# Kernel tuning notes

Hardware: AMD Instinct MI355X
Metric: run time of the kernel (lower is better)

## Reference

```python
import jax, jax.numpy as jnp
import numpy as np

N = 40000      # nodes
E = 640000     # edges
G = 2048       # graphs
D = 128        # emb_dim
T = 10         # num_tasks
L = 5          # layers
ATOM_VOCAB = 64
BOND_VOCAB = 8
BN_EPS = 1e-5


def _bn(x, g, b, m, v):
    # inference-mode BatchNorm1d with running stats
    return (x - m) * jax.lax.rsqrt(v + BN_EPS) * g + b


def setup_inputs() -> dict:
    key = jax.random.key(0)
    ks = jax.random.split(key, 24)
    inp = {
        "x_atom": jax.random.randint(ks[0], (N, 9), 0, ATOM_VOCAB),
        "edge_index": jax.random.randint(ks[1], (2, E), 0, N),
        "edge_attr": jax.random.randint(ks[2], (E, 3), 0, BOND_VOCAB),
        "batch": jnp.sort(jax.random.randint(ks[3], (N,), 0, G)),
        # embedding tables
        "atom_emb": jax.random.normal(ks[4], (9, ATOM_VOCAB, D)) * 0.1,
        "bond_emb": jax.random.normal(ks[5], (L, 3, BOND_VOCAB, D)) * 0.1,
        # per-layer GIN params (stacked over L)
        "eps": jnp.zeros((L,)),
        "W1": jax.random.normal(ks[6], (L, D, 2 * D)) * 0.05,
        "b1": jnp.zeros((L, 2 * D)),
        "g1": jnp.ones((L, 2 * D)),
        "bt1": jnp.zeros((L, 2 * D)),
        "m1": jax.random.normal(ks[7], (L, 2 * D)) * 0.1,
        "v1": jax.random.uniform(ks[8], (L, 2 * D), minval=0.5, maxval=1.5),
        "W2": jax.random.normal(ks[9], (L, 2 * D, D)) * 0.05,
        "b2": jnp.zeros((L, D)),
        # outer BatchNorm per layer
        "gO": jnp.ones((L, D)),
        "btO": jnp.zeros((L, D)),
        "mO": jax.random.normal(ks[10], (L, D)) * 0.1,
        "vO": jax.random.uniform(ks[11], (L, D), minval=0.5, maxval=1.5),
        # prediction head
        "Wp": jax.random.normal(ks[12], (D, T)) * 0.05,
        "bp": jnp.zeros((T,)),
    }
    return inp


def reference(x_atom, edge_index, edge_attr, batch, atom_emb, bond_emb, eps,
              W1, b1, g1, bt1, m1, v1, W2, b2, gO, btO, mO, vO, Wp, bp):
    src, dst = edge_index[0], edge_index[1]
    # AtomEncoder: sum of per-feature embeddings -> [N, D]
    x = atom_emb[jnp.arange(9)[None, :], x_atom].sum(axis=1)
    feat3 = jnp.arange(3)[None, :]
    for i in range(L):
        # BondEncoder for this layer -> [E, D]
        e = bond_emb[i][feat3, edge_attr].sum(axis=1)
        # message: relu(x_j + edge_emb); aggregate: scatter-add at dst
        msg = jax.nn.relu(x[src] + e)
        agg = jax.ops.segment_sum(msg, dst, num_segments=N)
        h = (1.0 + eps[i]) * x + agg
        # MLP: Linear -> BN -> ReLU -> Linear
        h = jax.nn.relu(_bn(h @ W1[i] + b1[i], g1[i], bt1[i], m1[i], v1[i]))
        h = h @ W2[i] + b2[i]
        # outer BN; ReLU after all but last layer (dropout = identity in eval)
        x = _bn(h, gO[i], btO[i], mO[i], vO[i])
        if i < L - 1:
            x = jax.nn.relu(x)
    # global mean pool over graphs
    sums = jax.ops.segment_sum(x, batch, num_segments=G)
    cnt = jax.ops.segment_sum(jnp.ones((N,), x.dtype), batch, num_segments=G)
    pooled = sums / jnp.maximum(cnt, 1.0)[:, None]
    return pooled @ Wp + bp
```

## Files before the change

### kernel.cpp

```cpp
#include <hip/hip_runtime.h>
#include <hip/hip_bf16.h>

#define NN 40000
#define NE 640000
#define NG 2048
#define DD 128
#define NT 10
#define NL 5
#define NB 80

typedef __attribute__((ext_vector_type(8))) short short8;
typedef __attribute__((ext_vector_type(4))) float f32x4;
typedef unsigned short ushort_t;

static __device__ __forceinline__ ushort_t f2b(float f) {
    return __bfloat16_as_ushort(__float2bfloat16(f));
}
static __device__ __forceinline__ float b2f(ushort_t u) {
    return __bfloat162float(__ushort_as_bfloat16(u));
}

__global__ void __launch_bounds__(256)
k_setup(const float* __restrict__ W1, const float* __restrict__ W2,
        const float* __restrict__ bemb, const int* __restrict__ xa,
        const float* __restrict__ aemb, const int* __restrict__ ei,
        ushort_t* __restrict__ W1P, ushort_t* __restrict__ W2P,
        ushort_t* __restrict__ ebsum16, ushort_t* __restrict__ x16,
        int* __restrict__ deg) {
    int b = blockIdx.x, t = threadIdx.x;
    if (b < 1280) {
        int tid = b * 256 + t;
        int layer = tid >> 16;
        int r = tid & 65535;
        int half = r >> 15;
        int q = r & 32767;
        int j = q & 7;
        int lane = (q >> 3) & 63;
        if (half == 0) {
            int kk = (q >> 9) & 3;
            int nt = q >> 11;
            int n = nt * 16 + (lane & 15);
            int k = kk * 32 + (lane >> 4) * 8 + j;
            W1P[layer * 32768 + q] = f2b(W1[(layer * DD + k) * 256 + n]);
        } else {
            int kk = (q >> 9) & 7;
            int nt = q >> 12;
            int n = nt * 16 + (lane & 15);
            int k = kk * 32 + (lane >> 4) * 8 + j;
            W2P[layer * 32768 + q] = f2b(W2[(layer * 256 + k) * DD + n]);
        }
        int d = tid & 127;
        int c = (tid >> 7) & 511;
        const float* bl = bemb + (size_t)layer * 3 * 8 * DD;
        ebsum16[tid] = f2b(bl[(c & 7) * DD + d] + bl[(8 + ((c >> 3) & 7)) * DD + d] +
                           bl[(16 + (c >> 6)) * DD + d]);
    } else if (b < 21280) {
        int half = t >> 7, d = t & 127;
        int n = (b - 1280) * 2 + half;
        __shared__ int idx[2][9];
        if (d < 9) idx[half][d] = xa[n * 9 + d];
        __syncthreads();
        float s = 0.f;
#pragma unroll
        for (int f = 0; f < 9; ++f) s += aemb[(f * 64 + idx[half][f]) * DD + d];
        x16[n * DD + d] = f2b(s);
    } else {
        int e = (b - 21280) * 256 + t;
        atomicAdd(&deg[ei[NE + e]], 1);
    }
}


__global__ void k_scan1(const int* __restrict__ deg, int* __restrict__ off,
                        int* __restrict__ blksum) {
    int b = blockIdx.x, t = threadIdx.x;
    int i = b * 256 + t;
    __shared__ int s[256];
    int v = (i < NN) ? deg[i] : 0;
    s[t] = v;
    __syncthreads();
    for (int d = 1; d < 256; d <<= 1) {
        int add = (t >= d) ? s[t - d] : 0;
        __syncthreads();
        s[t] += add;
        __syncthreads();
    }
    if (i <= NN) off[i] = s[t] - v;
    if (t == 255) blksum[b] = s[255];
}

__global__ void k_scan2(int* __restrict__ blk) {
    int t = threadIdx.x;
    __shared__ int s[256];
    int v = blk[t];
    s[t] = v;
    __syncthreads();
    for (int d = 1; d < 256; d <<= 1) {
        int add = (t >= d) ? s[t - d] : 0;
        __syncthreads();
        s[t] += add;
        __syncthreads();
    }
    blk[256 + t] = s[t] - v;
}

__global__ void k_scan3(int* __restrict__ off, const int* __restrict__ blk) {
    int b = blockIdx.x, t = threadIdx.x;
    int i = b * 256 + t;
    if (i <= NN) off[i] += blk[256 + b];
}

__global__ void __launch_bounds__(256)
k_bucket(const int* __restrict__ ei, const int* __restrict__ ea,
         const int* __restrict__ off, int* __restrict__ gbk,
         int2* __restrict__ ebuf) {
    __shared__ int hist[NB];
    __shared__ int sbase[NB];
    int t = threadIdx.x;
    int e0 = blockIdx.x * 1024;
    if (t < NB) hist[t] = 0;
    __syncthreads();
    int rank[4], buck[4], rec[4], dstv[4];
#pragma unroll
    for (int k = 0; k < 4; ++k) {
        int e = e0 + k * 256 + t;
        int src = ei[e];
        int dst = ei[NE + e];
        int a0 = ea[e * 3 + 0], a1 = ea[e * 3 + 1], a2 = ea[e * 3 + 2];
        rec[k] = src | ((a0 | (a1 << 3) | (a2 << 6)) << 16);
        dstv[k] = dst;
        int b = dst >> 9;
        buck[k] = b;
        rank[k] = atomicAdd(&hist[b], 1);
    }
    __syncthreads();
    if (t < NB) sbase[t] = atomicAdd(&gbk[t], hist[t]);
    __syncthreads();
#pragma unroll
    for (int k = 0; k < 4; ++k) {
        int b = buck[k];
        int slot = off[b << 9] + sbase[b] + rank[k];
        ebuf[slot] = make_int2(rec[k], dstv[k]);
    }
}

__global__ void k_scatter2(const int2* __restrict__ ebuf, const int* __restrict__ off,
                           int* __restrict__ cursor, int2* __restrict__ epack) {
    int i = blockIdx.x * 256 + threadIdx.x;
    int2 s = ebuf[i];
    int dst = s.y;
    int p = off[dst] + atomicAdd(&cursor[dst], 1);
    epack[p] = make_int2(s.x & 0xFFFF, s.x >> 16);
}

__global__ void __launch_bounds__(256)
k_gather(const ushort_t* __restrict__ xin, const int* __restrict__ off,
         const int2* __restrict__ epack, const ushort_t* __restrict__ ebsum16,
         const float* __restrict__ eps, int layer, ushort_t* __restrict__ h16) {
    int t = threadIdx.x;
    int lane = t & 63;
    int n = blockIdx.x * 4 + (t >> 6);
    const ushort2* x2 = (const ushort2*)xin;
    const ushort2* eb2 = (const ushort2*)ebsum16;
    ushort2 xv = x2[n * 64 + lane];
    float es = 1.f + eps[layer];
    float ax = es * b2f(xv.x), ay = es * b2f(xv.y);
    int p = off[n], p1 = off[n + 1];

    if (p < p1) {
        int2 e[8];
#pragma unroll
        for (int j = 0; j < 8; ++j) e[j] = epack[(p + j < p1) ? p + j : p1 - 1];
        while (p < p1) {
            int np = p + 8;
            int2 f[8];
            bool nh = np < p1;
            if (nh) {
#pragma unroll
                for (int j = 0; j < 8; ++j) f[j] = epack[(np + j < p1) ? np + j : p1 - 1];
            }
            ushort2 v[8], s[8];
#pragma unroll
            for (int j = 0; j < 8; ++j) {
                v[j] = eb2[e[j].y * 64 + lane];
                s[j] = x2[e[j].x * 64 + lane];
            }
#pragma unroll
            for (int j = 0; j < 8; ++j) {
                if (p + j < p1) {
                    ax += fmaxf(b2f(v[j].x) + b2f(s[j].x), 0.f);
                    ay += fmaxf(b2f(v[j].y) + b2f(s[j].y), 0.f);
                }
            }
#pragma unroll
            for (int j = 0; j < 8; ++j) e[j] = f[j];
            p = np;
        }
    }
    ushort2 o;
    o.x = f2b(ax);
    o.y = f2b(ay);
    ((ushort2*)h16)[n * 64 + lane] = o;
}

__global__ void __launch_bounds__(256)
k_mlp_mfma(const ushort_t* __restrict__ h16, const ushort_t* __restrict__ W1P,
           const ushort_t* __restrict__ W2P, const float* __restrict__ b1,
           const float* __restrict__ g1, const float* __restrict__ bt1,
           const float* __restrict__ m1, const float* __restrict__ v1,
           const float* __restrict__ b2_, const float* __restrict__ gO,
           const float* __restrict__ btO, const float* __restrict__ mO,
           const float* __restrict__ vO, int relu, ushort_t* __restrict__ xout) {
    __shared__ ushort_t aS[32 * 136];
    __shared__ ushort_t mid[32 * 264];
    int t = threadIdx.x;
    int wave = t >> 6, lane = t & 63;
    int row0 = blockIdx.x * 32;
    int lrow = lane & 15, quad = lane >> 4;

#pragma unroll
    for (int ps = 0; ps < 2; ++ps) {
        int idx = ps * 256 + t;
        int r = idx >> 4, c = (idx & 15) * 8;
        *(short8*)&aS[r * 136 + c] = *(const short8*)&h16[(row0 + r) * DD + c];
    }
    __syncthreads();

    f32x4 acc1[2][4];
#pragma unroll
    for (int rt = 0; rt < 2; ++rt)
#pragma unroll
        for (int i = 0; i < 4; ++i) acc1[rt][i] = (f32x4){0.f, 0.f, 0.f, 0.f};
#pragma unroll
    for (int kk = 0; kk < 4; ++kk) {
        short8 af0 = *(const short8*)&aS[lrow * 136 + kk * 32 + quad * 8];
        short8 af1 = *(const short8*)&aS[(16 + lrow) * 136 + kk * 32 + quad * 8];
#pragma unroll
        for (int i = 0; i < 4; ++i) {
            int nt = wave * 4 + i;
            short8 bf = *(const short8*)&W1P[((nt * 4 + kk) * 64 + lane) * 8];
            acc1[0][i] = __builtin_amdgcn_mfma_f32_16x16x32_bf16(af0, bf, acc1[0][i], 0, 0, 0);
            acc1[1][i] = __builtin_amdgcn_mfma_f32_16x16x32_bf16(af1, bf, acc1[1][i], 0, 0, 0);
        }
    }
#pragma unroll
    for (int i = 0; i < 4; ++i) {
        int col = (wave * 4 + i) * 16 + lrow;
        float s1 = g1[col] * rsqrtf(v1[col] + 1e-5f);
        float sh = bt1[col] - (m1[col] - b1[col]) * s1;
#pragma unroll
        for (int rt = 0; rt < 2; ++rt)
#pragma unroll
            for (int r = 0; r < 4; ++r) {
                int row = rt * 16 + quad * 4 + r;
                float o = acc1[rt][i][r] * s1 + sh;
                mid[row * 264 + col] = f2b(fmaxf(o, 0.f));
            }
    }
    __syncthreads();

    f32x4 acc2[2][2];
#pragma unroll
    for (int rt = 0; rt < 2; ++rt)
#pragma unroll
        for (int i = 0; i < 2; ++i) acc2[rt][i] = (f32x4){0.f, 0.f, 0.f, 0.f};
#pragma unroll
    for (int kk = 0; kk < 8; ++kk) {
        short8 af0 = *(const short8*)&mid[lrow * 264 + kk * 32 + quad * 8];
        short8 af1 = *(const short8*)&mid[(16 + lrow) * 264 + kk * 32 + quad * 8];
#pragma unroll
        for (int i = 0; i < 2; ++i) {
            int nt = wave * 2 + i;
            short8 bf = *(const short8*)&W2P[((nt * 8 + kk) * 64 + lane) * 8];
            acc2[0][i] = __builtin_amdgcn_mfma_f32_16x16x32_bf16(af0, bf, acc2[0][i], 0, 0, 0);
            acc2[1][i] = __builtin_amdgcn_mfma_f32_16x16x32_bf16(af1, bf, acc2[1][i], 0, 0, 0);
        }
    }
#pragma unroll
    for (int i = 0; i < 2; ++i) {
        int col = (wave * 2 + i) * 16 + lrow;
        float s = gO[col] * rsqrtf(vO[col] + 1e-5f);
        float sh = btO[col] - (mO[col] - b2_[col]) * s;
#pragma unroll
        for (int rt = 0; rt < 2; ++rt)
#pragma unroll
            for (int r = 0; r < 4; ++r) {
                int row = rt * 16 + quad * 4 + r;
                float o = acc2[rt][i][r] * s + sh;
                if (relu) o = fmaxf(o, 0.f);
                xout[(row0 + row) * DD + col] = f2b(o);
            }
    }
}

__global__ void k_poolhead(const ushort_t* __restrict__ x16,
                           const int* __restrict__ batch,
                           const float* __restrict__ Wp, const float* __restrict__ bp,
                           float* __restrict__ out) {
    int g = blockIdx.x, d = threadIdx.x;
    int lo = 0, hi = NN;
    while (lo < hi) { int m = (lo + hi) >> 1; if (batch[m] < g) lo = m + 1; else hi = m; }
    int start = lo;
    hi = NN;
    while (lo < hi) { int m = (lo + hi) >> 1; if (batch[m] < g + 1) lo = m + 1; else hi = m; }
    int end = lo;
    float s = 0.f;
    for (int n = start; n < end; ++n) s += b2f(x16[n * DD + d]);
    float c = fmaxf((float)(end - start), 1.f);
    __shared__ float p[DD];
    p[d] = s / c;
    __syncthreads();
    if (d < NT) {
        float acc = bp[d];
#pragma unroll 8
        for (int k = 0; k < DD; ++k) acc = fmaf(p[k], Wp[k * NT + d], acc);
        out[g * NT + d] = acc;
    }
}

extern "C" void kernel_launch(void* const* d_in, const int* in_sizes, int n_in,
                              void* d_out, int out_size, void* d_ws, size_t ws_size,
                              hipStream_t stream) {
    const int* x_atom = (const int*)d_in[0];
    const int* edge_index = (const int*)d_in[1];
    const int* edge_attr = (const int*)d_in[2];
    const int* batch = (const int*)d_in[3];
    const float* atom_emb = (const float*)d_in[4];
    const float* bond_emb = (const float*)d_in[5];
    const float* eps = (const float*)d_in[6];
    const float* W1 = (const float*)d_in[7];
    const float* b1 = (const float*)d_in[8];
    const float* g1 = (const float*)d_in[9];
    const float* bt1 = (const float*)d_in[10];
    const float* m1 = (const float*)d_in[11];
    const float* v1 = (const float*)d_in[12];
    const float* W2 = (const float*)d_in[13];
    const float* b2 = (const float*)d_in[14];
    const float* gO = (const float*)d_in[15];
    const float* btO = (const float*)d_in[16];
    const float* mO = (const float*)d_in[17];
    const float* vO = (const float*)d_in[18];
    const float* Wp = (const float*)d_in[19];
    const float* bp = (const float*)d_in[20];

    ushort_t* x16a = (ushort_t*)d_ws;
    ushort_t* x16b = x16a + NN * DD;
    ushort_t* h16 = x16b + NN * DD;
    ushort_t* W1P = h16 + NN * DD;
    ushort_t* W2P = W1P + NL * 32768;
    ushort_t* ebsum16 = W2P + NL * 32768;
    int* deg = (int*)(ebsum16 + NL * 65536);
    int* off = deg + NN;
    int* blk = off + 40064;
    int* cursor = blk + 512;
    int* gbk = cursor + NN;
    int2* epack = (int2*)(gbk + 128);
    int2* ebuf = epack + NE;

    hipMemsetAsync(deg, 0, (NN + 40064 + 512 + NN + 128) * sizeof(int), stream);

    k_setup<<<23780, 256, 0, stream>>>(W1, W2, bond_emb, x_atom, atom_emb,
                                       edge_index, W1P, W2P, ebsum16, x16a, deg);
    k_scan1<<<157, 256, 0, stream>>>(deg, off, blk);
    k_scan2<<<1, 256, 0, stream>>>(blk);
    k_scan3<<<157, 256, 0, stream>>>(off, blk);
    k_bucket<<<NE / 1024, 256, 0, stream>>>(edge_index, edge_attr, off, gbk, ebuf);
    k_scatter2<<<NE / 256, 256, 0, stream>>>(ebuf, off, cursor, epack);

    for (int i = 0; i < NL; ++i) {
        ushort_t* xin = (i & 1) ? x16b : x16a;
        ushort_t* xout = (i & 1) ? x16a : x16b;
        k_gather<<<NN / 4, 256, 0, stream>>>(xin, off, epack, ebsum16 + i * 65536,
                                             eps, i, h16);
        k_mlp_mfma<<<NN / 32, 256, 0, stream>>>(
            h16, W1P + (size_t)i * 32768, W2P + (size_t)i * 32768, b1 + i * 256,
            g1 + i * 256, bt1 + i * 256, m1 + i * 256, v1 + i * 256, b2 + i * DD,
            gO + i * DD, btO + i * DD, mO + i * DD, vO + i * DD,
            (i < NL - 1) ? 1 : 0, xout);
    }
    k_poolhead<<<NG, DD, 0, stream>>>(x16b, batch, Wp, bp, (float*)d_out);
}
```

Baseline: 470.1 us.

## Gather two edges per wave with 8-byte loads and fuse scan into one kernel

The gather kernel now splits each 64-lane wave into two halves. Each half processes a different edge with 8-byte (4 bf16) loads per lane, doubling bytes per load instruction and edges in flight. The halves are combined with a cross-lane shuffle before the self term is added. A tail loop handles edge counts that are not a multiple of 8. Separately, the three-kernel prefix scan is replaced by a single 1024-thread block scan, removing two launches at the cost of a serial per-thread segment.

```diff
diff --git a/kernel.cpp b/kernel.cpp
--- a/kernel.cpp
+++ b/kernel.cpp
@@ -18,6 +18,12 @@
 }
 static __device__ __forceinline__ float b2f(ushort_t u) {
     return __bfloat162float(__ushort_as_bfloat16(u));
+}
+static __device__ __forceinline__ float blo(unsigned u) {
+    return __bfloat162float(__ushort_as_bfloat16((ushort_t)(u & 0xFFFF)));
+}
+static __device__ __forceinline__ float bhi(unsigned u) {
+    return __bfloat162float(__ushort_as_bfloat16((ushort_t)(u >> 16)));
 }
 
 __global__ void __launch_bounds__(256)
@@ -71,43 +77,34 @@
 }
 
 
-__global__ void k_scan1(const int* __restrict__ deg, int* __restrict__ off,
-                        int* __restrict__ blksum) {
-    int b = blockIdx.x, t = threadIdx.x;
-    int i = b * 256 + t;
-    __shared__ int s[256];
-    int v = (i < NN) ? deg[i] : 0;
-    s[t] = v;
-    __syncthreads();
-    for (int d = 1; d < 256; d <<= 1) {
+__global__ void __launch_bounds__(1024)
+k_scan(const int* __restrict__ deg, int* __restrict__ off) {
+    int t = threadIdx.x;
+    int base = t * 40;
+    int v[40];
+    int sum = 0;
+#pragma unroll 8
+    for (int i = 0; i < 40; ++i) {
+        int idx = base + i;
+        int d = (idx < NN) ? deg[idx] : 0;
+        v[i] = sum;
+        sum += d;
+    }
+    __shared__ int s[1024];
+    s[t] = sum;
+    __syncthreads();
+    for (int d = 1; d < 1024; d <<= 1) {
         int add = (t >= d) ? s[t - d] : 0;
         __syncthreads();
         s[t] += add;
         __syncthreads();
     }
-    if (i <= NN) off[i] = s[t] - v;
-    if (t == 255) blksum[b] = s[255];
-}
-
-__global__ void k_scan2(int* __restrict__ blk) {
-    int t = threadIdx.x;
-    __shared__ int s[256];
-    int v = blk[t];
-    s[t] = v;
-    __syncthreads();
-    for (int d = 1; d < 256; d <<= 1) {
-        int add = (t >= d) ? s[t - d] : 0;
-        __syncthreads();
-        s[t] += add;
-        __syncthreads();
-    }
-    blk[256 + t] = s[t] - v;
-}
-
-__global__ void k_scan3(int* __restrict__ off, const int* __restrict__ blk) {
-    int b = blockIdx.x, t = threadIdx.x;
-    int i = b * 256 + t;
-    if (i <= NN) off[i] += blk[256 + b];
+    int excl = s[t] - sum;
+#pragma unroll 8
+    for (int i = 0; i < 40; ++i) {
+        int idx = base + i;
+        if (idx <= NN) off[idx] = excl + v[i];
+    }
 }
 
 __global__ void __launch_bounds__(256)
@@ -155,52 +152,77 @@
 
 __global__ void __launch_bounds__(256)
 k_gather(const ushort_t* __restrict__ xin, const int* __restrict__ off,
-         const int2* __restrict__ epack, const ushort_t* __restrict__ ebsum16,
+         const int2* __restrict__ epack, const ushort_t* __restrict__ eb,
          const float* __restrict__ eps, int layer, ushort_t* __restrict__ h16) {
     int t = threadIdx.x;
     int lane = t & 63;
+    int half = lane >> 5;
+    int l32 = lane & 31;
     int n = blockIdx.x * 4 + (t >> 6);
-    const ushort2* x2 = (const ushort2*)xin;
-    const ushort2* eb2 = (const ushort2*)ebsum16;
-    ushort2 xv = x2[n * 64 + lane];
+    const uint2* xq = (const uint2*)xin;
+    const uint2* ebq = (const uint2*)eb;
+    float a0 = 0.f, a1 = 0.f, a2 = 0.f, a3 = 0.f;
+    int p = off[n], p1 = off[n + 1];
+
+    int2 e[8];
+    bool have = (p + 8 <= p1);
+    if (have) {
+#pragma unroll
+        for (int j = 0; j < 8; ++j) e[j] = epack[p + j];
+    }
+    while (have) {
+        int np = p + 8;
+        bool nh = (np + 8 <= p1);
+        int2 f[8];
+        if (nh) {
+#pragma unroll
+            for (int j = 0; j < 8; ++j) f[j] = epack[np + j];
+        }
+#pragma unroll
+        for (int j = 0; j < 4; ++j) {
+            int2 ep = half ? e[2 * j + 1] : e[2 * j];
+            uint2 xr = xq[ep.x * 32 + l32];
+            uint2 er = ebq[ep.y * 32 + l32];
+            a0 += fmaxf(blo(xr.x) + blo(er.x), 0.f);
+            a1 += fmaxf(bhi(xr.x) + bhi(er.x), 0.f);
+            a2 += fmaxf(blo(xr.y) + blo(er.y), 0.f);
+            a3 += fmaxf(bhi(xr.y) + bhi(er.y), 0.f);
+        }
+#pragma unroll
+        for (int j = 0; j < 8; ++j) e[j] = f[j];
+        p = np;
+        have = nh;
+    }
+    while (p < p1) {
+        int iA = p, iB = (p + 1 < p1) ? (p + 1) : p;
+        int2 ep = half ? epack[iB] : epack[iA];
+        bool valid = half ? (p + 1 < p1) : true;
+        uint2 xr = xq[ep.x * 32 + l32];
+        uint2 er = ebq[ep.y * 32 + l32];
+        if (valid) {
+            a0 += fmaxf(blo(xr.x) + blo(er.x), 0.f);
+            a1 += fmaxf(bhi(xr.x) + bhi(er.x), 0.f);
+            a2 += fmaxf(blo(xr.y) + blo(er.y), 0.f);
+            a3 += fmaxf(bhi(xr.y) + bhi(er.y), 0.f);
+        }
+        p += 2;
+    }
+    a0 += __shfl_xor(a0, 32);
+    a1 += __shfl_xor(a1, 32);
+    a2 += __shfl_xor(a2, 32);
+    a3 += __shfl_xor(a3, 32);
     float es = 1.f + eps[layer];
-    float ax = es * b2f(xv.x), ay = es * b2f(xv.y);
-    int p = off[n], p1 = off[n + 1];
-
-    if (p < p1) {
-        int2 e[8];
-#pragma unroll
-        for (int j = 0; j < 8; ++j) e[j] = epack[(p + j < p1) ? p + j : p1 - 1];
-        while (p < p1) {
-            int np = p + 8;
-            int2 f[8];
-            bool nh = np < p1;
-            if (nh) {
-#pragma unroll
-                for (int j = 0; j < 8; ++j) f[j] = epack[(np + j < p1) ? np + j : p1 - 1];
-            }
-            ushort2 v[8], s[8];
-#pragma unroll
-            for (int j = 0; j < 8; ++j) {
-                v[j] = eb2[e[j].y * 64 + lane];
-                s[j] = x2[e[j].x * 64 + lane];
-            }
-#pragma unroll
-            for (int j = 0; j < 8; ++j) {
-                if (p + j < p1) {
-                    ax += fmaxf(b2f(v[j].x) + b2f(s[j].x), 0.f);
-                    ay += fmaxf(b2f(v[j].y) + b2f(s[j].y), 0.f);
-                }
-            }
-#pragma unroll
-            for (int j = 0; j < 8; ++j) e[j] = f[j];
-            p = np;
-        }
-    }
-    ushort2 o;
-    o.x = f2b(ax);
-    o.y = f2b(ay);
-    ((ushort2*)h16)[n * 64 + lane] = o;
+    uint2 xb = xq[n * 32 + l32];
+    a0 += es * blo(xb.x);
+    a1 += es * bhi(xb.x);
+    a2 += es * blo(xb.y);
+    a3 += es * bhi(xb.y);
+    if (half == 0) {
+        uint2 o;
+        o.x = (unsigned)f2b(a0) | ((unsigned)f2b(a1) << 16);
+        o.y = (unsigned)f2b(a2) | ((unsigned)f2b(a3) << 16);
+        ((uint2*)h16)[n * 32 + l32] = o;
+    }
 }
 
 __global__ void __launch_bounds__(256)
@@ -351,19 +373,16 @@
     ushort_t* ebsum16 = W2P + NL * 32768;
     int* deg = (int*)(ebsum16 + NL * 65536);
     int* off = deg + NN;
-    int* blk = off + 40064;
-    int* cursor = blk + 512;
+    int* cursor = off + 40064;
     int* gbk = cursor + NN;
     int2* epack = (int2*)(gbk + 128);
     int2* ebuf = epack + NE;
 
-    hipMemsetAsync(deg, 0, (NN + 40064 + 512 + NN + 128) * sizeof(int), stream);
+    hipMemsetAsync(deg, 0, (NN + 40064 + NN + 128) * sizeof(int), stream);
 
     k_setup<<<23780, 256, 0, stream>>>(W1, W2, bond_emb, x_atom, atom_emb,
                                        edge_index, W1P, W2P, ebsum16, x16a, deg);
-    k_scan1<<<157, 256, 0, stream>>>(deg, off, blk);
-    k_scan2<<<1, 256, 0, stream>>>(blk);
-    k_scan3<<<157, 256, 0, stream>>>(off, blk);
+    k_scan<<<1, 1024, 0, stream>>>(deg, off);
     k_bucket<<<NE / 1024, 256, 0, stream>>>(edge_index, edge_attr, off, gbk, ebuf);
     k_scatter2<<<NE / 256, 256, 0, stream>>>(ebuf, off, cursor, epack);
 
```

Measured after the change: 664.5 us. +41.4%, slower.
